# Kernel tuning notes

Measured on AMD Instinct MI355X. Metric: run time of the kernel, lower is better.

Reference implementation:

```python
import jax, jax.numpy as jnp
import numpy as np

WEIGHT = 4.0
SIGMA_DATA = 16.0
ALPHA_DNA = 5.0
ALPHA_RNA = 5.0
ALPHA_LIG = 10.0
EPS = 1e-6
D, L, NTOK = 4, 4096, 512


def setup_inputs() -> dict:
    key = jax.random.key(0)
    ks = jax.random.split(key, 8)
    X_L = jax.random.normal(ks[0], (D, L, 3), dtype=jnp.float32)
    X_gt_L = jax.random.normal(ks[1], (1, L, 3), dtype=jnp.float32)
    crd_mask_L = jax.random.randint(ks[2], (1, L), 0, 2).astype(bool)
    is_dna = jax.random.randint(ks[3], (NTOK,), 0, 2).astype(bool)
    is_rna = jax.random.randint(ks[4], (NTOK,), 0, 2).astype(bool)
    is_ligand = jax.random.randint(ks[5], (NTOK,), 0, 2).astype(bool)
    tok_idx = jnp.sort(jax.random.randint(ks[6], (L,), 0, NTOK, dtype=jnp.int64))
    t = jax.random.uniform(ks[7], (D,), dtype=jnp.float32)
    return {"X_L": X_L, "X_gt_L": X_gt_L, "crd_mask_L": crd_mask_L,
            "is_dna": is_dna, "is_rna": is_rna, "is_ligand": is_ligand,
            "tok_idx": tok_idx, "t": t}


def _smoothed_lddt(X_L, X_gt, crd_mask_L, is_dna, is_rna, tok_idx):
    # X_gt: nan_to_num'd ground truth, shape [1, L, 3]
    n = X_L.shape[1]
    fi, si = jnp.triu_indices(n, k=1)  # P pairs
    gt_d = jnp.linalg.norm(X_gt[0, fi] - X_gt[0, si], axis=-1)  # [P]
    is_na = (is_dna | is_rna)[tok_idx][fi]
    cutoff = jnp.where(is_na, 30.0, 15.0)
    pm = (gt_d > 0) & (gt_d < cutoff)
    pm = pm & crd_mask_L[0, fi] & crd_mask_L[0, si]
    pm = pm & (tok_idx[fi] != tok_idx[si])
    pmf = pm.astype(X_L.dtype)  # [P]
    pred_d = jnp.linalg.norm(X_L[:, fi] - X_L[:, si], axis=-1)  # [D, P]
    delta = jnp.abs(pred_d - gt_d[None, :] + EPS)
    s = (jax.nn.sigmoid(0.5 - delta) + jax.nn.sigmoid(1.0 - delta)
         + jax.nn.sigmoid(2.0 - delta) + jax.nn.sigmoid(4.0 - delta))
    lddt = 0.25 * jnp.sum(s * pmf[None, :], axis=1) / (jnp.sum(pmf) + EPS)
    return 1.0 - lddt  # [D]


def reference(X_L, X_gt_L, crd_mask_L, is_dna, is_rna, is_ligand, tok_idx, t):
    dtype = X_L.dtype
    mask = crd_mask_L.astype(dtype)  # [1, L]
    alpha = (is_dna * ALPHA_DNA + is_rna * ALPHA_RNA + is_ligand * ALPHA_LIG)
    w_L = (1.0 + alpha[tok_idx]).astype(dtype)[None, :] * mask  # [1,L]->[D,L] by bcast
    X_gt = jnp.nan_to_num(X_gt_L)
    sq = jnp.sum((X_L - X_gt) ** 2, axis=-1)  # [D, L]
    l_mse = (1.0 / 3.0) * jnp.sum(w_L * sq, axis=-1) / (jnp.sum(mask[0]) + 1e-4)
    lam = (t ** 2 + SIGMA_DATA ** 2) / ((t * SIGMA_DATA) ** 2)  # edm_lambda
    l_diff = jnp.minimum(lam * l_mse, 2.0)  # clamp_diffusion_loss
    lddt_loss = _smoothed_lddt(X_L, X_gt, crd_mask_L, is_dna, is_rna, tok_idx)
    total = jnp.mean(l_diff) + jnp.mean(lddt_loss)
    return WEIGHT * total
```

## Files before the change

kernel.cpp:

```cpp
#include <hip/hip_runtime.h>

#define LPTS 4096
#define NTOKS 512
#define TILE 32
#define CAP (LPTS + TILE)
#define GRID_B 2080
#define PREP_B 16

#define OFF_GT 512
#define OFF_PX (OFF_GT + CAP * 16)
#define OFF_PY (OFF_PX + CAP * 16)
#define OFF_PZ (OFF_PY + CAP * 16)
#define OFF_PART (OFF_PZ + CAP * 16)

static __device__ __forceinline__ float nan0(float x) {
  if (!(x == x)) return 0.f;
  return fminf(fmaxf(x, -3.402823466e38f), 3.402823466e38f);
}

static __device__ __forceinline__ float sterm(float dx, float dy, float dz, float tmp) {
  float d2 = fmaf(dx, dx, fmaf(dy, dy, dz * dz));
  float pd = __builtin_amdgcn_sqrtf(d2);
  float delta = fminf(fabsf(pd + tmp), 25.f);
  float e = __expf(delta);
  float e2 = e * e;
  float e3 = e2 * e;
  float e4 = e2 * e2;
  float Nn = fmaf(0.0366994762f, e3, fmaf(0.7506558488f, e2, fmaf(3.3841830690f, e, 4.f)));
  float Dd = fmaf(0.00055308437f, e4,
             fmaf(0.0366994762f, e3, fmaf(0.3753279244f, e2, fmaf(1.1280610231f, e, 1.f))));
  return Nn * __builtin_amdgcn_rcpf(Dd);
}

__global__ __launch_bounds__(256) void prep_kernel(
    const float* __restrict__ XL, const float* __restrict__ Xgt,
    const void* __restrict__ crd, const void* __restrict__ dna,
    const void* __restrict__ rna, const void* __restrict__ lig,
    const void* __restrict__ tok, float* __restrict__ ws) {
  int b = blockIdx.x, t = threadIdx.x;
  int l = b * 256 + t;
  int* wsi = (int*)ws;
  const int* toki = (const int*)tok;
  const int* crdi = (const int*)crd;
  const unsigned char* crdB = (const unsigned char*)crd;
  __shared__ int sflags[5];
  if (t < 5) sflags[t] = 0;
  __syncthreads();
  {
    int f0 = 0;
    for (int i = t; i < LPTS / 2; i += 256) f0 |= (toki[2 * i + 1] != 0);
    if (f0) atomicOr(&sflags[0], 1);
    int f1 = 0;
    for (int i = t; i < LPTS / 4; i += 256) f1 |= ((unsigned)crdi[i] > 1u);
    if (f1) atomicOr(&sflags[1], 1);
    if (t < NTOKS / 4) {
      if ((unsigned)((const int*)dna)[t] > 1u) atomicOr(&sflags[2], 1);
      if ((unsigned)((const int*)rna)[t] > 1u) atomicOr(&sflags[3], 1);
      if ((unsigned)((const int*)lig)[t] > 1u) atomicOr(&sflags[4], 1);
    }
  }
  __syncthreads();
  bool tok64 = sflags[0] == 0;
  bool crdb = sflags[1] != 0, dnab = sflags[2] != 0,
       rnab = sflags[3] != 0, ligb = sflags[4] != 0;

  int pre = 0;
  for (int i = t; i < b * 256; i += 256)
    pre += crdb ? (crdB[i] != 0) : (crdi[i] != 0);

  int tk = tok64 ? toki[2 * l] : toki[l];
  int tki = min(max(tk, 0), NTOKS - 1);
  int m  = crdb ? (crdB[l] != 0) : (crdi[l] != 0);
  int dn = (dnab ? (int)((const unsigned char*)dna)[tki] : ((const int*)dna)[tki]) != 0;
  int rn = (rnab ? (int)((const unsigned char*)rna)[tki] : ((const int*)rna)[tki]) != 0;
  int lg = (ligb ? (int)((const unsigned char*)lig)[tki] : ((const int*)lig)[tki]) != 0;
  float w = (1.f + 5.f * dn + 5.f * rn + 10.f * lg) * (float)m;
  float gx = nan0(Xgt[3 * l + 0]);
  float gy = nan0(Xgt[3 * l + 1]);
  float gz = nan0(Xgt[3 * l + 2]);
  int meta = (tk & 0xFFFF) | (1 << 16) | ((dn | rn) << 17);
  float xs[4], ys[4], zs[4];
  float v[5];
#pragma unroll
  for (int d = 0; d < 4; ++d) {
    xs[d] = XL[(d * LPTS + l) * 3 + 0];
    ys[d] = XL[(d * LPTS + l) * 3 + 1];
    zs[d] = XL[(d * LPTS + l) * 3 + 2];
    float dx = xs[d] - gx, dy = ys[d] - gy, dz = zs[d] - gz;
    v[d] = w * (dx * dx + dy * dy + dz * dz);
  }
  v[4] = (float)m;

  int lane = t & 63, wid = t >> 6;
  unsigned long long bal = __ballot(m != 0);
  int p = pre;
#pragma unroll
  for (int off = 32; off; off >>= 1) p += __shfl_down(p, off, 64);
  __shared__ int sw[4], wcnt[4];
  if (lane == 0) { sw[wid] = p; wcnt[wid] = __popcll(bal); }
  __syncthreads();
  int block_base = sw[0] + sw[1] + sw[2] + sw[3];
  int wbase = block_base;
  for (int q = 0; q < wid; ++q) wbase += wcnt[q];
  int pos = wbase + __popcll(bal & ((1ull << lane) - 1ull));
  float4* cgt4 = (float4*)((char*)ws + OFF_GT);
  float4* cpx  = (float4*)((char*)ws + OFF_PX);
  float4* cpy  = (float4*)((char*)ws + OFF_PY);
  float4* cpz  = (float4*)((char*)ws + OFF_PZ);
  if (m) {
    cgt4[pos] = make_float4(gx, gy, gz, __int_as_float(meta));
    cpx[pos] = make_float4(xs[0], xs[1], xs[2], xs[3]);
    cpy[pos] = make_float4(ys[0], ys[1], ys[2], ys[3]);
    cpz[pos] = make_float4(zs[0], zs[1], zs[2], zs[3]);
  }
  if (b == PREP_B - 1 && t == 0)
    wsi[5] = block_base + wcnt[0] + wcnt[1] + wcnt[2] + wcnt[3];

#pragma unroll
  for (int k = 0; k < 5; ++k) {
    float x = v[k];
#pragma unroll
    for (int off = 32; off; off >>= 1) x += __shfl_down(x, off, 64);
    v[k] = x;
  }
  __shared__ float bred[4][5];
  if (lane == 0)
    for (int k = 0; k < 5; ++k) bred[wid][k] = v[k];
  __syncthreads();
  if (t == 0)
    for (int k = 0; k < 5; ++k)
      ws[8 + b * 5 + k] = bred[0][k] + bred[1][k] + bred[2][k] + bred[3][k];
}

__global__ __launch_bounds__(256) void pair_kernel(float* __restrict__ ws) {
  const int* wsi = (const int*)ws;
  const int Lv = wsi[5];
  const int NT = (Lv + TILE - 1) >> 5;
  const int NA = NT * (NT + 1) / 2;
  const float4* cgt4 = (const float4*)((const char*)ws + OFF_GT);
  const float4* cpx  = (const float4*)((const char*)ws + OFF_PX);
  const float4* cpy  = (const float4*)((const char*)ws + OFF_PY);
  const float4* cpz  = (const float4*)((const char*)ws + OFF_PZ);
  __shared__ float4 sg[TILE], sx[TILE], sy[TILE], sz[TILE];
  __shared__ float bred[4][5];
  int t = threadIdx.x;
  int r = t & 31, g = t >> 5;
  float a0 = 0.f, a1 = 0.f, a2 = 0.f, a3 = 0.f, a4 = 0.f;
  for (int b = blockIdx.x; b < NA; b += GRID_B) {
    int tj = (int)((__builtin_amdgcn_sqrtf(8.f * (float)b + 1.f) - 1.f) * 0.5f);
    while ((tj + 1) * (tj + 2) / 2 <= b) ++tj;
    while (tj * (tj + 1) / 2 > b) --tj;
    int ti = b - tj * (tj + 1) / 2;
    int i0 = ti * TILE, j0 = tj * TILE;
    __syncthreads();
    if (t < 32) {
      float4 gv = cgt4[j0 + t];
      if (j0 + t >= Lv) gv.w = __int_as_float(0);
      sg[t] = gv;
    } else if (t < 64) sx[t - 32] = cpx[j0 + t - 32];
    else if (t < 96) sy[t - 64] = cpy[j0 + t - 64];
    else if (t < 128) sz[t - 96] = cpz[j0 + t - 96];
    __syncthreads();
    int i = i0 + r;
    float4 rg = cgt4[i], rx = cpx[i], ry = cpy[i], rz = cpz[i];
    int rmeta = __float_as_int(rg.w);
    int rtok = rmeta & 0xFFFF;
    bool rm = (i < Lv);
    float cutoff = ((rmeta >> 17) & 1) ? 30.f : 15.f;
    bool diag = (ti == tj);
#pragma unroll
    for (int k = 0; k < 4; ++k) {
      int jj = g * 4 + k;
      float4 cg = sg[jj];
      int cmeta = __float_as_int(cg.w);
      float dgx = rg.x - cg.x, dgy = rg.y - cg.y, dgz = rg.z - cg.z;
      float gd = __builtin_amdgcn_sqrtf(fmaf(dgx, dgx, fmaf(dgy, dgy, dgz * dgz)));
      bool pm = rm && ((cmeta >> 16) & 1) && (gd > 0.f) && (gd < cutoff) &&
                (rtok != (cmeta & 0xFFFF));
      if (diag) pm = pm && (j0 + jj > i);
      float pmf = pm ? 1.f : 0.f;
      float tmp = 1e-6f - gd;
      float4 cx = sx[jj], cy = sy[jj], cz = sz[jj];
      float s0 = sterm(rx.x - cx.x, ry.x - cy.x, rz.x - cz.x, tmp);
      float s1 = sterm(rx.y - cx.y, ry.y - cy.y, rz.y - cz.y, tmp);
      float s2 = sterm(rx.z - cx.z, ry.z - cy.z, rz.z - cz.z, tmp);
      float s3 = sterm(rx.w - cx.w, ry.w - cy.w, rz.w - cz.w, tmp);
      a0 = fmaf(s0, pmf, a0);
      a1 = fmaf(s1, pmf, a1);
      a2 = fmaf(s2, pmf, a2);
      a3 = fmaf(s3, pmf, a3);
      a4 += pmf;
    }
  }
  float v[5] = {a0, a1, a2, a3, a4};
#pragma unroll
  for (int k = 0; k < 5; ++k) {
    float x = v[k];
#pragma unroll
    for (int off = 32; off; off >>= 1) x += __shfl_down(x, off, 64);
    v[k] = x;
  }
  int wid = t >> 6, lane = t & 63;
  if (lane == 0)
    for (int k = 0; k < 5; ++k) bred[wid][k] = v[k];
  __syncthreads();
  if (t == 0) {
    float* part = (float*)((char*)ws + OFF_PART);
#pragma unroll
    for (int k = 0; k < 5; ++k)
      part[blockIdx.x * 5 + k] = bred[0][k] + bred[1][k] + bred[2][k] + bred[3][k];
  }
}

__global__ __launch_bounds__(256) void final_kernel(
    const float* __restrict__ ws, const float* __restrict__ t_in,
    float* __restrict__ out) {
  int t = threadIdx.x;
  const float* part = (const float*)((const char*)ws + OFF_PART);
  float u[5] = {0.f, 0.f, 0.f, 0.f, 0.f};
  for (int i = t; i < GRID_B; i += 256) {
#pragma unroll
    for (int k = 0; k < 5; ++k) u[k] += part[i * 5 + k];
  }
#pragma unroll
  for (int k = 0; k < 5; ++k) {
    float x = u[k];
#pragma unroll
    for (int off = 32; off; off >>= 1) x += __shfl_down(x, off, 64);
    u[k] = x;
  }
  __shared__ float bred[4][5];
  int wid = t >> 6, lane = t & 63;
  if (lane == 0)
    for (int k = 0; k < 5; ++k) bred[wid][k] = u[k];
  __syncthreads();
  if (t == 0) {
    float ssum[5];
#pragma unroll
    for (int k = 0; k < 5; ++k)
      ssum[k] = bred[0][k] + bred[1][k] + bred[2][k] + bred[3][k];
    float mse[4] = {0.f, 0.f, 0.f, 0.f};
    float mask_sum = 0.f;
    for (int b = 0; b < PREP_B; ++b) {
#pragma unroll
      for (int d = 0; d < 4; ++d) mse[d] += ws[8 + b * 5 + d];
      mask_sum += ws[8 + b * 5 + 4];
    }
    float pm_sum = ssum[4];
    float tot = 0.f;
#pragma unroll
    for (int d = 0; d < 4; ++d) {
      float lmse = (mse[d] * (1.f / 3.f)) / (mask_sum + 1e-4f);
      float td = t_in[d];
      float lam = (td * td + 256.f) / (256.f * td * td);
      float ldiff = fminf(lam * lmse, 2.f);
      float lddt = 0.25f * ssum[d] / (pm_sum + 1e-6f);
      tot += 0.25f * (ldiff + (1.f - lddt));
    }
    out[0] = 4.f * tot;
  }
}

extern "C" void kernel_launch(void* const* d_in, const int* in_sizes, int n_in,
                              void* d_out, int out_size, void* d_ws, size_t ws_size,
                              hipStream_t stream) {
  (void)in_sizes; (void)n_in; (void)out_size; (void)ws_size;
  const float* XL  = (const float*)d_in[0];
  const float* Xgt = (const float*)d_in[1];
  float* ws = (float*)d_ws;
  float* out = (float*)d_out;
  prep_kernel<<<PREP_B, 256, 0, stream>>>(XL, Xgt, d_in[2], d_in[3], d_in[4],
                                          d_in[5], d_in[6], ws);
  pair_kernel<<<GRID_B, 256, 0, stream>>>(ws);
  final_kernel<<<1, 256, 0, stream>>>(ws, (const float*)d_in[7], out);
}
```

Before: 27.27 us.

## Prescale coordinates by log2e, pad with sentinels, and halve pair-kernel block size

The prep kernel now stores all ground-truth and predicted coordinates multiplied by log2(e), so each sigmoid term can call exp2 directly instead of __expf. The clamp, epsilon and cutoff constants are scaled to match. The prep kernel also writes 32 sentinel entries past the valid count: huge coordinates and a unique meta word. That lets the pair kernel drop the row-validity and column-mask checks and replace the token and mask tests with a single meta-word inequality. The pair kernel runs 128-thread blocks that each cover 8 columns per thread rather than 4, which raises per-thread work and cuts per-block overhead but halves resident threads per block.

```diff
diff --git a/kernel.cpp b/kernel.cpp
--- a/kernel.cpp
+++ b/kernel.cpp
@@ -7,6 +7,13 @@
 #define GRID_B 2080
 #define PREP_B 16
 
+#define LOG2E   1.44269504f
+#define EPS_S   (1e-6f * LOG2E)
+#define CLAMP_S (25.f * LOG2E)
+#define CUT15_S (15.f * LOG2E)
+#define CUT30_S (30.f * LOG2E)
+#define PAD_BIG 1e15f
+
 #define OFF_GT 512
 #define OFF_PX (OFF_GT + CAP * 16)
 #define OFF_PY (OFF_PX + CAP * 16)
@@ -21,8 +28,8 @@
 static __device__ __forceinline__ float sterm(float dx, float dy, float dz, float tmp) {
   float d2 = fmaf(dx, dx, fmaf(dy, dy, dz * dz));
   float pd = __builtin_amdgcn_sqrtf(d2);
-  float delta = fminf(fabsf(pd + tmp), 25.f);
-  float e = __expf(delta);
+  float delta = fminf(fabsf(pd + tmp), CLAMP_S);
+  float e = __builtin_amdgcn_exp2f(delta);
   float e2 = e * e;
   float e3 = e2 * e;
   float e4 = e2 * e2;
@@ -78,7 +85,7 @@
   float gx = nan0(Xgt[3 * l + 0]);
   float gy = nan0(Xgt[3 * l + 1]);
   float gz = nan0(Xgt[3 * l + 2]);
-  int meta = (tk & 0xFFFF) | (1 << 16) | ((dn | rn) << 17);
+  int meta = (tk & 0xFFFF) | ((dn | rn) << 16);
   float xs[4], ys[4], zs[4];
   float v[5];
 #pragma unroll
@@ -108,14 +115,20 @@
   float4* cpy  = (float4*)((char*)ws + OFF_PY);
   float4* cpz  = (float4*)((char*)ws + OFF_PZ);
   if (m) {
-    cgt4[pos] = make_float4(gx, gy, gz, __int_as_float(meta));
-    cpx[pos] = make_float4(xs[0], xs[1], xs[2], xs[3]);
-    cpy[pos] = make_float4(ys[0], ys[1], ys[2], ys[3]);
-    cpz[pos] = make_float4(zs[0], zs[1], zs[2], zs[3]);
-  }
-  if (b == PREP_B - 1 && t == 0)
-    wsi[5] = block_base + wcnt[0] + wcnt[1] + wcnt[2] + wcnt[3];
-
+    cgt4[pos] = make_float4(gx * LOG2E, gy * LOG2E, gz * LOG2E, __int_as_float(meta));
+    cpx[pos] = make_float4(xs[0] * LOG2E, xs[1] * LOG2E, xs[2] * LOG2E, xs[3] * LOG2E);
+    cpy[pos] = make_float4(ys[0] * LOG2E, ys[1] * LOG2E, ys[2] * LOG2E, ys[3] * LOG2E);
+    cpz[pos] = make_float4(zs[0] * LOG2E, zs[1] * LOG2E, zs[2] * LOG2E, zs[3] * LOG2E);
+  }
+  if (b == PREP_B - 1) {
+    int Lv = block_base + wcnt[0] + wcnt[1] + wcnt[2] + wcnt[3];
+    if (t == 0) wsi[5] = Lv;
+    if (t < TILE) {
+      cgt4[Lv + t] = make_float4(PAD_BIG, PAD_BIG, PAD_BIG, __int_as_float(0x7FFFFFFF));
+      float4 z = make_float4(0.f, 0.f, 0.f, 0.f);
+      cpx[Lv + t] = z; cpy[Lv + t] = z; cpz[Lv + t] = z;
+    }
+  }
 #pragma unroll
   for (int k = 0; k < 5; ++k) {
     float x = v[k];
@@ -132,7 +145,7 @@
       ws[8 + b * 5 + k] = bred[0][k] + bred[1][k] + bred[2][k] + bred[3][k];
 }
 
-__global__ __launch_bounds__(256) void pair_kernel(float* __restrict__ ws) {
+__global__ __launch_bounds__(128) void pair_kernel(float* __restrict__ ws) {
   const int* wsi = (const int*)ws;
   const int Lv = wsi[5];
   const int NT = (Lv + TILE - 1) >> 5;
@@ -142,7 +155,7 @@
   const float4* cpy  = (const float4*)((const char*)ws + OFF_PY);
   const float4* cpz  = (const float4*)((const char*)ws + OFF_PZ);
   __shared__ float4 sg[TILE], sx[TILE], sy[TILE], sz[TILE];
-  __shared__ float bred[4][5];
+  __shared__ float bred[2][5];
   int t = threadIdx.x;
   int r = t & 31, g = t >> 5;
   float a0 = 0.f, a1 = 0.f, a2 = 0.f, a3 = 0.f, a4 = 0.f;
@@ -153,33 +166,26 @@
     int ti = b - tj * (tj + 1) / 2;
     int i0 = ti * TILE, j0 = tj * TILE;
     __syncthreads();
-    if (t < 32) {
-      float4 gv = cgt4[j0 + t];
-      if (j0 + t >= Lv) gv.w = __int_as_float(0);
-      sg[t] = gv;
-    } else if (t < 64) sx[t - 32] = cpx[j0 + t - 32];
+    if (t < 32) sg[t] = cgt4[j0 + t];
+    else if (t < 64) sx[t - 32] = cpx[j0 + t - 32];
     else if (t < 96) sy[t - 64] = cpy[j0 + t - 64];
-    else if (t < 128) sz[t - 96] = cpz[j0 + t - 96];
+    else sz[t - 96] = cpz[j0 + t - 96];
     __syncthreads();
     int i = i0 + r;
     float4 rg = cgt4[i], rx = cpx[i], ry = cpy[i], rz = cpz[i];
     int rmeta = __float_as_int(rg.w);
-    int rtok = rmeta & 0xFFFF;
-    bool rm = (i < Lv);
-    float cutoff = ((rmeta >> 17) & 1) ? 30.f : 15.f;
+    float cutoff = (rmeta & 0x10000) ? CUT30_S : CUT15_S;
     bool diag = (ti == tj);
 #pragma unroll
-    for (int k = 0; k < 4; ++k) {
-      int jj = g * 4 + k;
+    for (int k = 0; k < 8; ++k) {
+      int jj = g * 8 + k;
       float4 cg = sg[jj];
-      int cmeta = __float_as_int(cg.w);
       float dgx = rg.x - cg.x, dgy = rg.y - cg.y, dgz = rg.z - cg.z;
       float gd = __builtin_amdgcn_sqrtf(fmaf(dgx, dgx, fmaf(dgy, dgy, dgz * dgz)));
-      bool pm = rm && ((cmeta >> 16) & 1) && (gd > 0.f) && (gd < cutoff) &&
-                (rtok != (cmeta & 0xFFFF));
-      if (diag) pm = pm && (j0 + jj > i);
+      bool pm = (gd > 0.f) & (gd < cutoff) & (rmeta != __float_as_int(cg.w));
+      if (diag) pm = pm & (jj > r);
       float pmf = pm ? 1.f : 0.f;
-      float tmp = 1e-6f - gd;
+      float tmp = EPS_S - gd;
       float4 cx = sx[jj], cy = sy[jj], cz = sz[jj];
       float s0 = sterm(rx.x - cx.x, ry.x - cy.x, rz.x - cz.x, tmp);
       float s1 = sterm(rx.y - cx.y, ry.y - cy.y, rz.y - cz.y, tmp);
@@ -208,7 +214,7 @@
     float* part = (float*)((char*)ws + OFF_PART);
 #pragma unroll
     for (int k = 0; k < 5; ++k)
-      part[blockIdx.x * 5 + k] = bred[0][k] + bred[1][k] + bred[2][k] + bred[3][k];
+      part[blockIdx.x * 5 + k] = bred[0][k] + bred[1][k];
   }
 }
 
@@ -271,6 +277,6 @@
   float* out = (float*)d_out;
   prep_kernel<<<PREP_B, 256, 0, stream>>>(XL, Xgt, d_in[2], d_in[3], d_in[4],
                                           d_in[5], d_in[6], ws);
-  pair_kernel<<<GRID_B, 256, 0, stream>>>(ws);
+  pair_kernel<<<GRID_B, 128, 0, stream>>>(ws);
   final_kernel<<<1, 256, 0, stream>>>(ws, (const float*)d_in[7], out);
 }
```

Result: faster. 26.39 us (-3.3%).
